# Kernel tuning notes

Measured on AMD Instinct MI355X. Metric: run time of the kernel, lower is better.

## Reference

```python
import jax, jax.numpy as jnp
import numpy as np

B, S, D, K, R = 4, 2048, 2048, 8, 64


def setup_inputs() -> dict:
    key = jax.random.key(0)
    ks = jax.random.split(key, 7)
    x = jax.random.normal(ks[0], (B, S, D), dtype=jnp.float32)
    # low-rank expert factors: U_k (D,R), V_k (R,D), stacked over K
    U = jax.random.normal(ks[1], (K, D, R), dtype=jnp.float32) * 0.02
    V = jax.random.normal(ks[2], (K, R, D), dtype=jnp.float32) * 0.02
    # router MLP: Linear(D,D) -> ReLU -> Linear(D,K)
    W1 = jax.random.normal(ks[3], (D, D), dtype=jnp.float32) * 0.02
    b1 = jnp.zeros((D,), dtype=jnp.float32)
    W2 = jax.random.normal(ks[4], (D, K), dtype=jnp.float32) * 0.02
    b2 = jnp.zeros((K,), dtype=jnp.float32)
    return {"x": x, "U": U, "V": V, "W1": W1, "b1": b1, "W2": W2, "b2": b2}


def reference(x, U, V, W1, b1, W2, b2):
    # router: alpha = softmax(MLP(x)) over K experts
    h = jax.nn.relu(jnp.einsum('bsd,de->bse', x, W1) + b1)
    alpha = jax.nn.softmax(jnp.einsum('bse,ek->bsk', h, W2) + b2, axis=-1)  # [B,S,K]
    # T_eff @ x with T_eff = sum_k alpha_k * U_k V_k, computed in factored form
    vx = jnp.einsum('krd,bsd->bskr', V, x)       # [B,S,K,R]
    uvx = jnp.einsum('kdr,bskr->bskd', U, vx)    # [B,S,K,D]
    out = jnp.einsum('bsk,bskd->bsd', alpha, uvx)
    return out
```

## Files before the change

### kernel.cpp

```cpp
#include <hip/hip_runtime.h>

typedef unsigned short u16;
typedef unsigned int u32;
typedef __bf16 bf16x8 __attribute__((ext_vector_type(8)));
typedef float f32x4 __attribute__((ext_vector_type(4)));
typedef u16 u16x8 __attribute__((ext_vector_type(8)));

__device__ __forceinline__ u16 f2bf(float f) {
  u32 u = __builtin_bit_cast(u32, f);
  u += 0x7FFFu + ((u >> 16) & 1u);
  return (u16)(u >> 16);
}
__device__ __forceinline__ float bf2f(u16 h) {
  u32 u = ((u32)h) << 16;
  return __builtin_bit_cast(float, u);
}

#define GLD16(gp, lp)                                                      \
  __builtin_amdgcn_global_load_lds(                                        \
      (const __attribute__((address_space(1))) void*)(gp),                 \
      (__attribute__((address_space(3))) void*)(lp), 16, 0, 0)

#define LGKM0()                                          \
  do {                                                   \
    asm volatile("s_waitcnt lgkmcnt(0)" ::: "memory");   \
    __builtin_amdgcn_sched_barrier(0);                   \
  } while (0)
#define VMCNT(n)                                              \
  do {                                                        \
    asm volatile("s_waitcnt vmcnt(" #n ")" ::: "memory");     \
    __builtin_amdgcn_sched_barrier(0);                        \
  } while (0)
#define BAR() __builtin_amdgcn_s_barrier()

__global__ void cvt_f32_bf16(const float* __restrict__ in, u16* __restrict__ out, int n8) {
  int i = blockIdx.x * 256 + threadIdx.x;
  if (i >= n8) return;
  const float4* p = (const float4*)in + (size_t)i * 2;
  float4 a = p[0], b = p[1];
  u16x8 o;
  o[0] = f2bf(a.x); o[1] = f2bf(a.y); o[2] = f2bf(a.z); o[3] = f2bf(a.w);
  o[4] = f2bf(b.x); o[5] = f2bf(b.y); o[6] = f2bf(b.z); o[7] = f2bf(b.w);
  *((u16x8*)out + i) = o;
}

__global__ void transpose_cvt(const float* __restrict__ W1, u16* __restrict__ W1t) {
  __shared__ float tile[32][33];
  const int tx = threadIdx.x;
  const int ty = threadIdx.y;
  const int e0 = blockIdx.x * 32, d0 = blockIdx.y * 32;
#pragma unroll
  for (int j = 0; j < 4; ++j)
    tile[ty + j * 8][tx] = W1[(size_t)(d0 + ty + j * 8) * 2048 + e0 + tx];
  __syncthreads();
#pragma unroll
  for (int j = 0; j < 4; ++j)
    W1t[(size_t)(e0 + ty + j * 8) * 2048 + d0 + tx] = f2bf(tile[tx][ty + j * 8]);
}

__global__ void make_Ut(const float* __restrict__ U, u16* __restrict__ Ut) {
  int idx = blockIdx.x * 256 + threadIdx.x;
  int n = idx >> 9;
  int kr = idx & 511;
  int k = kr >> 6, r = kr & 63;
  Ut[idx] = f2bf(U[(size_t)k * 131072 + (size_t)n * 64 + r]);
}

template <int EPI>
__launch_bounds__(512, 2)
__global__ void gemm256(const u16* __restrict__ A, const u16* __restrict__ Bt,
                        float* __restrict__ Cf, u16* __restrict__ Cb,
                        const float* __restrict__ bias, int M, int N, int Kd) {
  __shared__ u16 lds[2][4][8192];

  const int nbx = N >> 8;
  const int nwg = (M >> 8) * nbx;
  int wg = blockIdx.x;
  wg = (wg & 7) * (nwg >> 3) + (wg >> 3);
  const int bx = wg % nbx, by = wg / nbx;
  const int bm = by << 8, bn = bx << 8;

  const int tid = threadIdx.x;
  const int lane = tid & 63, wave = tid >> 6;
  const int wr = wave >> 2;
  const int wc = wave & 3;
  const int hc = 2 + (wc >> 1);
  const int l15 = lane & 15, hi = lane >> 4;
  const int swz = l15 & 7;

  const int scol = ((tid & 7) ^ ((tid >> 3) & 7)) << 3;
  const size_t goff0 = (size_t)(tid >> 3) * Kd + scol;
  const size_t goff1 = goff0 + (size_t)64 * Kd;
  const int d0e = tid * 8, d1e = tid * 8 + 4096;

  const int NT = Kd >> 6;

  int aidx[8], bidx[4];
#pragma unroll
  for (int m = 0; m < 8; ++m) aidx[m] = (m * 16 + l15) * 64;
#pragma unroll
  for (int n = 0; n < 4; ++n) bidx[n] = ((wc & 1) * 64 + n * 16 + l15) * 64;
  const int slot0 = ((0 * 4 + hi) ^ swz) << 3;
  const int slot1 = ((1 * 4 + hi) ^ swz) << 3;

  f32x4 acc[8][4];
#pragma unroll
  for (int m = 0; m < 8; ++m)
#pragma unroll
    for (int n = 0; n < 4; ++n) acc[m][n] = f32x4{0.f, 0.f, 0.f, 0.f};

#define STAGE(tt, ht)                                                          \
  do {                                                                         \
    const u16* g_ = ((ht) < 2 ? A + (size_t)(bm + ((ht) & 1) * 128) * Kd       \
                              : Bt + (size_t)(bn + ((ht) & 1) * 128) * Kd)     \
                    + (size_t)(tt) * 64;                                       \
    u16* l_ = &lds[(tt) & 1][(ht)][0];                                         \
    GLD16(g_ + goff0, l_ + d0e);                                               \
    GLD16(g_ + goff1, l_ + d1e);                                               \
  } while (0)

#define MFMA2(av, bv, nA, nB)                                                  \
  _Pragma("unroll") for (int m = 0; m < 8; ++m) {                              \
    acc[m][nA] = __builtin_amdgcn_mfma_f32_16x16x32_bf16(av[m], bv[nA], acc[m][nA], 0, 0, 0); \
    acc[m][nB] = __builtin_amdgcn_mfma_f32_16x16x32_bf16(av[m], bv[nB], acc[m][nB], 0, 0, 0); \
  }

  STAGE(0, 0); STAGE(0, 1); STAGE(0, 2); STAGE(0, 3);
  STAGE(1, 0); STAGE(1, 1); STAGE(1, 2);
  VMCNT(6);
  BAR();

  for (int t = 0; t < NT; ++t) {
    const int b = t & 1;
    const u16* As = &lds[b][wr][0];
    const u16* Bs = &lds[b][hc][0];
    bf16x8 av0[8], bv0[4], av1[8], bv1[4];

#pragma unroll
    for (int m = 0; m < 8; ++m) av0[m] = *(const bf16x8*)(As + aidx[m] + slot0);
#pragma unroll
    for (int n = 0; n < 4; ++n) bv0[n] = *(const bf16x8*)(Bs + bidx[n] + slot0);
    if (t + 1 < NT) STAGE(t + 1, 3);
    BAR();
    LGKM0();
    __builtin_amdgcn_s_setprio(1);
    MFMA2(av0, bv0, 0, 1);
    __builtin_amdgcn_s_setprio(0);
    BAR();

#pragma unroll
    for (int m = 0; m < 8; ++m) av1[m] = *(const bf16x8*)(As + aidx[m] + slot1);
#pragma unroll
    for (int n = 0; n < 4; ++n) bv1[n] = *(const bf16x8*)(Bs + bidx[n] + slot1);
    BAR();
    LGKM0();
    __builtin_amdgcn_s_setprio(1);
    MFMA2(av0, bv0, 2, 3);
    __builtin_amdgcn_s_setprio(0);
    BAR();

    if (t + 2 < NT) { STAGE(t + 2, 0); STAGE(t + 2, 1); }
    BAR();
    __builtin_amdgcn_s_setprio(1);
    MFMA2(av1, bv1, 0, 1);
    __builtin_amdgcn_s_setprio(0);
    BAR();

    if (t + 2 < NT) STAGE(t + 2, 2);
    BAR();
    __builtin_amdgcn_s_setprio(1);
    MFMA2(av1, bv1, 2, 3);
    __builtin_amdgcn_s_setprio(0);
    if (t < NT - 2) { VMCNT(6); }
    else if (t == NT - 2) { VMCNT(0); }
    BAR();
  }
#undef STAGE
#undef MFMA2

#pragma unroll
  for (int m = 0; m < 8; ++m) {
    const int row0 = bm + wr * 128 + m * 16 + hi * 4;
#pragma unroll
    for (int n = 0; n < 4; ++n) {
      const int col = bn + wc * 64 + n * 16 + l15;
      f32x4 v = acc[m][n];
      if (EPI == 0) {
        const float bsv = bias[col];
#pragma unroll
        for (int j = 0; j < 4; ++j) {
          float tv = v[j] + bsv;
          tv = tv > 0.f ? tv : 0.f;
          Cb[(size_t)(row0 + j) * N + col] = f2bf(tv);
        }
      } else {
#pragma unroll
        for (int j = 0; j < 4; ++j)
          Cf[(size_t)(row0 + j) * N + col] = v[j];
      }
    }
  }
}

template <int EPI>
__launch_bounds__(256, 2)
__global__ void gemm_bt(const u16* __restrict__ A, const u16* __restrict__ Bt,
                        float* __restrict__ Cf, u16* __restrict__ Cb,
                        const float* __restrict__ bias, const float* __restrict__ alpha,
                        int M, int N, int Kd) {
  __shared__ u16 As[128 * 64];
  __shared__ u16 Bs[128 * 64];

  const int nbx = N >> 7;
  const int nwg = (M >> 7) * nbx;
  int wg = blockIdx.x;
  wg = (wg & 7) * (nwg >> 3) + (wg >> 3);
  const int bx = wg % nbx, by = wg / nbx;
  const int bm = by << 7, bn = bx << 7;

  const int tid = threadIdx.x;
  const int lane = tid & 63, wave = tid >> 6;
  const int wr = wave >> 1, wc = wave & 1;
  const int l15 = lane & 15, hi = lane >> 4;
  const int swz7 = l15 & 7;

  f32x4 acc[4][4];
#pragma unroll
  for (int m = 0; m < 4; ++m)
#pragma unroll
    for (int n = 0; n < 4; ++n)
      acc[m][n] = f32x4{0.f, 0.f, 0.f, 0.f};

  const int srow = tid >> 3;
  const int swzc = ((tid & 7) ^ (srow & 7)) << 3;
  const size_t ldsBase = (size_t)wave * 64 * 8;

  int aBase[4], bBase[4];
#pragma unroll
  for (int m = 0; m < 4; ++m) {
    aBase[m] = (wr * 64 + m * 16 + l15) * 64;
    bBase[m] = (wc * 64 + m * 16 + l15) * 64;
  }

  const u16* Ag = A + (size_t)(bm + srow) * Kd + swzc;
  const u16* Bg = Bt + (size_t)(bn + srow) * Kd + swzc;

  for (int k0 = 0; k0 < Kd; k0 += 64) {
#pragma unroll
    for (int i = 0; i < 4; ++i) {
      GLD16(Ag + (size_t)(i * 32) * Kd + k0, (u16*)As + i * 2048 + ldsBase);
      GLD16(Bg + (size_t)(i * 32) * Kd + k0, (u16*)Bs + i * 2048 + ldsBase);
    }
    __syncthreads();
#pragma unroll
    for (int kk = 0; kk < 2; ++kk) {
      const int soff = ((kk * 4 + hi) ^ swz7) << 3;
      bf16x8 av[4], bv[4];
#pragma unroll
      for (int m = 0; m < 4; ++m) av[m] = *(const bf16x8*)(As + aBase[m] + soff);
#pragma unroll
      for (int n = 0; n < 4; ++n) bv[n] = *(const bf16x8*)(Bs + bBase[n] + soff);
#pragma unroll
      for (int m = 0; m < 4; ++m)
#pragma unroll
        for (int n = 0; n < 4; ++n)
          acc[m][n] = __builtin_amdgcn_mfma_f32_16x16x32_bf16(av[m], bv[n], acc[m][n], 0, 0, 0);
    }
    __syncthreads();
  }

#pragma unroll
  for (int m = 0; m < 4; ++m) {
    const int row0 = bm + wr * 64 + m * 16 + hi * 4;
#pragma unroll
    for (int n = 0; n < 4; ++n) {
      const int col = bn + wc * 64 + n * 16 + l15;
      f32x4 v = acc[m][n];
      if (EPI == 1) {
        const int e = col >> 6;
#pragma unroll
        for (int j = 0; j < 4; ++j) {
          float t = v[j] * alpha[(size_t)(row0 + j) * 8 + e];
          Cb[(size_t)(row0 + j) * N + col] = f2bf(t);
        }
      } else {
#pragma unroll
        for (int j = 0; j < 4; ++j)
          Cf[(size_t)(row0 + j) * N + col] = v[j];
      }
    }
  }
}

__global__ void router(const u16* __restrict__ hb, const float* __restrict__ W2,
                       const float* __restrict__ b2, float* __restrict__ alphaOut) {
  const int row = blockIdx.x * 4 + (threadIdx.x >> 6);
  const int lane = threadIdx.x & 63;
  const u16* h = hb + (size_t)row * 2048;
  float a8[8] = {0.f, 0.f, 0.f, 0.f, 0.f, 0.f, 0.f, 0.f};
#pragma unroll
  for (int it = 0; it < 4; ++it) {
    const int d0 = it * 512 + lane * 8;
    u16x8 hv = *(const u16x8*)(h + d0);
#pragma unroll
    for (int jj = 0; jj < 8; ++jj) {
      const float hf = bf2f(hv[jj]);
      const float4* wp = (const float4*)(W2 + (size_t)(d0 + jj) * 8);
      float4 w0 = wp[0], w1 = wp[1];
      a8[0] += hf * w0.x; a8[1] += hf * w0.y; a8[2] += hf * w0.z; a8[3] += hf * w0.w;
      a8[4] += hf * w1.x; a8[5] += hf * w1.y; a8[6] += hf * w1.z; a8[7] += hf * w1.w;
    }
  }
#pragma unroll
  for (int off = 32; off; off >>= 1)
#pragma unroll
    for (int e = 0; e < 8; ++e) a8[e] += __shfl_xor(a8[e], off);
  if (lane == 0) {
    float mx = -1e30f;
#pragma unroll
    for (int e = 0; e < 8; ++e) { a8[e] += b2[e]; mx = a8[e] > mx ? a8[e] : mx; }
    float s = 0.f;
#pragma unroll
    for (int e = 0; e < 8; ++e) { a8[e] = __expf(a8[e] - mx); s += a8[e]; }
    const float inv = 1.f / s;
#pragma unroll
    for (int e = 0; e < 8; ++e) alphaOut[(size_t)row * 8 + e] = a8[e] * inv;
  }
}

extern "C" void kernel_launch(void* const* d_in, const int* in_sizes, int n_in,
                              void* d_out, int out_size, void* d_ws, size_t ws_size,
                              hipStream_t stream) {
  const float* x  = (const float*)d_in[0];
  const float* U  = (const float*)d_in[1];
  const float* V  = (const float*)d_in[2];
  const float* W1 = (const float*)d_in[3];
  const float* b1 = (const float*)d_in[4];
  const float* W2 = (const float*)d_in[5];
  const float* b2 = (const float*)d_in[6];
  float* out = (float*)d_out;

  char* w = (char*)d_ws;
  u16* xb   = (u16*)w; w += (size_t)16777216 * 2;
  u16* W1t  = (u16*)w; w += (size_t)4194304 * 2;
  u16* hb   = (u16*)w; w += (size_t)16777216 * 2;
  u16* Vb   = (u16*)w; w += (size_t)1048576 * 2;
  u16* Ut   = (u16*)w; w += (size_t)1048576 * 2;
  u16* wb   = (u16*)w; w += (size_t)4194304 * 2;
  float* alpha = (float*)w;

  cvt_f32_bf16<<<8192, 256, 0, stream>>>(x, xb, 2097152);
  cvt_f32_bf16<<<512, 256, 0, stream>>>(V, Vb, 131072);
  transpose_cvt<<<dim3(64, 64), dim3(32, 8), 0, stream>>>(W1, W1t);
  make_Ut<<<4096, 256, 0, stream>>>(U, Ut);

  gemm256<0><<<256, 512, 0, stream>>>(xb, W1t, nullptr, hb, b1, 8192, 2048, 2048);
  router<<<2048, 256, 0, stream>>>(hb, W2, b2, alpha);
  gemm_bt<1><<<256, 256, 0, stream>>>(xb, Vb, nullptr, wb, nullptr, alpha, 8192, 512, 2048);
  gemm256<2><<<256, 512, 0, stream>>>(wb, Ut, out, nullptr, nullptr, 8192, 2048, 512);
}
```

Baseline: 336.2 us.

## Restructure GEMM main loop into two-phase register-prefetch pipeline with one barrier

Replaces the four-barrier-per-half-tile MFMA schedule with a two-phase loop. Each phase issues all 32 MFMAs for one K-slot while the LDS fragments for the next slot or tile are already being read into registers. All four global-to-LDS stages of tile t+2 are now issued together right after a single barrier, instead of being spread across the iteration. This cuts synchronisation and scheduling overhead, but the loop now waits on VMCNT(0) every iteration, so it has less slack to hide global-load latency and holds more registers for the prefetched fragments.

```diff
diff --git a/kernel.cpp b/kernel.cpp
--- a/kernel.cpp
+++ b/kernel.cpp
@@ -119,64 +119,60 @@
     GLD16(g_ + goff1, l_ + d1e);                                               \
   } while (0)
 
-#define MFMA2(av, bv, nA, nB)                                                  \
-  _Pragma("unroll") for (int m = 0; m < 8; ++m) {                              \
-    acc[m][nA] = __builtin_amdgcn_mfma_f32_16x16x32_bf16(av[m], bv[nA], acc[m][nA], 0, 0, 0); \
-    acc[m][nB] = __builtin_amdgcn_mfma_f32_16x16x32_bf16(av[m], bv[nB], acc[m][nB], 0, 0, 0); \
-  }
+#define MFMA_ALL(av, bv)                                                       \
+  _Pragma("unroll") for (int m = 0; m < 8; ++m)                                \
+    _Pragma("unroll") for (int n = 0; n < 4; ++n)                              \
+      acc[m][n] = __builtin_amdgcn_mfma_f32_16x16x32_bf16(av[m], bv[n], acc[m][n], 0, 0, 0);
+
+  bf16x8 av0[8], bv0[4], av1[8], bv1[4];
 
   STAGE(0, 0); STAGE(0, 1); STAGE(0, 2); STAGE(0, 3);
-  STAGE(1, 0); STAGE(1, 1); STAGE(1, 2);
-  VMCNT(6);
+  STAGE(1, 0); STAGE(1, 1); STAGE(1, 2); STAGE(1, 3);
+  VMCNT(8);
   BAR();
+  __builtin_amdgcn_sched_barrier(0);
+  {
+    const u16* As = &lds[0][wr][0];
+    const u16* Bs = &lds[0][hc][0];
+#pragma unroll
+    for (int m = 0; m < 8; ++m) av0[m] = *(const bf16x8*)(As + aidx[m] + slot0);
+#pragma unroll
+    for (int n = 0; n < 4; ++n) bv0[n] = *(const bf16x8*)(Bs + bidx[n] + slot0);
+  }
 
   for (int t = 0; t < NT; ++t) {
     const int b = t & 1;
     const u16* As = &lds[b][wr][0];
     const u16* Bs = &lds[b][hc][0];
-    bf16x8 av0[8], bv0[4], av1[8], bv1[4];
-
-#pragma unroll
-    for (int m = 0; m < 8; ++m) av0[m] = *(const bf16x8*)(As + aidx[m] + slot0);
-#pragma unroll
-    for (int n = 0; n < 4; ++n) bv0[n] = *(const bf16x8*)(Bs + bidx[n] + slot0);
-    if (t + 1 < NT) STAGE(t + 1, 3);
+
+#pragma unroll
+    for (int m = 0; m < 8; ++m) av1[m] = *(const bf16x8*)(As + aidx[m] + slot1);
+#pragma unroll
+    for (int n = 0; n < 4; ++n) bv1[n] = *(const bf16x8*)(Bs + bidx[n] + slot1);
+    __builtin_amdgcn_s_setprio(1);
+    MFMA_ALL(av0, bv0);
+    __builtin_amdgcn_s_setprio(0);
+
+    LGKM0();
+    VMCNT(0);
     BAR();
-    LGKM0();
+    __builtin_amdgcn_sched_barrier(0);
+
+    if (t + 2 < NT) { STAGE(t + 2, 0); STAGE(t + 2, 1); STAGE(t + 2, 2); STAGE(t + 2, 3); }
+    if (t + 1 < NT) {
+      const u16* As2 = &lds[b ^ 1][wr][0];
+      const u16* Bs2 = &lds[b ^ 1][hc][0];
+#pragma unroll
+      for (int m = 0; m < 8; ++m) av0[m] = *(const bf16x8*)(As2 + aidx[m] + slot0);
+#pragma unroll
+      for (int n = 0; n < 4; ++n) bv0[n] = *(const bf16x8*)(Bs2 + bidx[n] + slot0);
+    }
     __builtin_amdgcn_s_setprio(1);
-    MFMA2(av0, bv0, 0, 1);
+    MFMA_ALL(av1, bv1);
     __builtin_amdgcn_s_setprio(0);
-    BAR();
-
-#pragma unroll
-    for (int m = 0; m < 8; ++m) av1[m] = *(const bf16x8*)(As + aidx[m] + slot1);
-#pragma unroll
-    for (int n = 0; n < 4; ++n) bv1[n] = *(const bf16x8*)(Bs + bidx[n] + slot1);
-    BAR();
-    LGKM0();
-    __builtin_amdgcn_s_setprio(1);
-    MFMA2(av0, bv0, 2, 3);
-    __builtin_amdgcn_s_setprio(0);
-    BAR();
-
-    if (t + 2 < NT) { STAGE(t + 2, 0); STAGE(t + 2, 1); }
-    BAR();
-    __builtin_amdgcn_s_setprio(1);
-    MFMA2(av1, bv1, 0, 1);
-    __builtin_amdgcn_s_setprio(0);
-    BAR();
-
-    if (t + 2 < NT) STAGE(t + 2, 2);
-    BAR();
-    __builtin_amdgcn_s_setprio(1);
-    MFMA2(av1, bv1, 2, 3);
-    __builtin_amdgcn_s_setprio(0);
-    if (t < NT - 2) { VMCNT(6); }
-    else if (t == NT - 2) { VMCNT(0); }
-    BAR();
   }
 #undef STAGE
-#undef MFMA2
+#undef MFMA_ALL
 
 #pragma unroll
   for (int m = 0; m < 8; ++m) {
```

Measured after the change: 325.2 us. 1.03x faster.
